# Optimization experiments

Hardware: AMD Instinct MI355X
Metric: run time of the kernel (lower is better)

Reference implementation:

```python
import jax, jax.numpy as jnp
import numpy as np


def setup_inputs() -> dict:
    key = jax.random.key(0)
    k1, k2, k3 = jax.random.split(key, 3)
    B, C, Z, S, T, H = 8, 128, 4, 8, 1024, 64
    WQ = jax.random.normal(k1, (C, Z, S, H), dtype=jnp.float32)
    WK = jax.random.normal(k2, (B, Z, T, H), dtype=jnp.float32)
    K = jax.random.normal(k3, (B, Z, T, H), dtype=jnp.float32)
    return {"WQ": WQ, "WK": WK, "K": K}


def reference(WQ, WK, K):
    # tanh non-linearities on keys (WQ is used raw, as in the original)
    WKt = jnp.tanh(WK)          # [b,z,t,h]
    Kt = jnp.tanh(K)            # [b,z,t,h]
    # attention scores per (batch, code, group, synonym) over tokens t
    scores = jnp.einsum('bzth,czsh->bczst', WKt, WQ)   # [b,c,z,s,t]
    attn = jax.nn.softmax(scores, axis=-1)             # softmax over t
    # weighted sum of (tanh'd) values over tokens
    context = jnp.einsum('bzth,bczst->bczsh', Kt, attn)  # [b,c,z,s,h]
    # AvgPool3d((1, s, 1)) then squeeze(-2) == mean over synonym axis s
    context = jnp.mean(context, axis=3)                  # [b,c,z,h]
    return (scores, context, attn)
```

## Files before the change

kernel.cpp:

```cpp
#include <hip/hip_runtime.h>

typedef _Float16 f16;
typedef f16 f16x4 __attribute__((ext_vector_type(4)));
typedef f16 f16x8 __attribute__((ext_vector_type(8)));
typedef float f32x16 __attribute__((ext_vector_type(16)));

#define NB 8
#define NC 128
#define NZ 4
#define NS 8
#define NT 1024
#define NH 64

#define WQ_N (NC*NZ*NS*NH)
#define WK_N (NB*NZ*NT*NH)

#define OUT_CTX  (NB*NC*NZ*NS*NT)
#define OUT_ATTN (OUT_CTX + NB*NC*NZ*NH)

__device__ __forceinline__ float fast_tanh(float x) {
    float e = __expf(2.0f * x);
    return 1.0f - 2.0f * __builtin_amdgcn_rcpf(e + 1.0f);
}

__global__ __launch_bounds__(256) void prep_kernel(
    const float* __restrict__ WQ, const float* __restrict__ WK, const float* __restrict__ K,
    f16* __restrict__ wqh, f16* __restrict__ wkh, f16* __restrict__ ktT)
{
    __shared__ f16 ldsT[64*64];
    const int tid = threadIdx.x;
    const int blk = blockIdx.x;
    if (blk < 512) {
        const int bz = blk >> 4;
        const int t0 = (blk & 15) << 6;
        #pragma unroll
        for (int it = 0; it < 4; ++it) {
            int idx = it*256 + tid;
            int tl  = idx >> 4;
            int seg = idx & 15;
            int gi  = (bz*NT + t0 + tl)*NH + seg*4;
            float4 wk4 = *(const float4*)(WK + gi);
            float4 k4  = *(const float4*)(K  + gi);
            f16x4 wv;
            wv[0] = (f16)fast_tanh(wk4.x);
            wv[1] = (f16)fast_tanh(wk4.y);
            wv[2] = (f16)fast_tanh(wk4.z);
            wv[3] = (f16)fast_tanh(wk4.w);
            *(f16x4*)(wkh + gi) = wv;
            ldsT[(seg*4+0)*64 + tl] = (f16)fast_tanh(k4.x);
            ldsT[(seg*4+1)*64 + tl] = (f16)fast_tanh(k4.y);
            ldsT[(seg*4+2)*64 + tl] = (f16)fast_tanh(k4.z);
            ldsT[(seg*4+3)*64 + tl] = (f16)fast_tanh(k4.w);
        }
        __syncthreads();
        #pragma unroll
        for (int it = 0; it < 4; ++it) {
            int idx = it*256 + tid;
            int h  = idx >> 4;
            int ts = idx & 15;
            f16x4 v = *(const f16x4*)&ldsT[h*64 + ts*4];
            *(f16x4*)(ktT + (bz*NH + h)*NT + t0 + ts*4) = v;
        }
    } else {
        const int ib = blk - 512;
        #pragma unroll
        for (int it = 0; it < 16; ++it) {
            int gi = ib*16384 + it*1024 + tid*4;
            float4 q = *(const float4*)(WQ + gi);
            f16x4 w;
            w[0] = (f16)q.x; w[1] = (f16)q.y; w[2] = (f16)q.z; w[3] = (f16)q.w;
            *(f16x4*)(wqh + gi) = w;
        }
    }
}

__global__ __launch_bounds__(256, 2) void fused_kernel(
    const f16* __restrict__ wqh, const f16* __restrict__ wkh, const f16* __restrict__ ktT,
    float* __restrict__ scores, float* __restrict__ attn, float* __restrict__ ctxout)
{
    __shared__ float rsL[4][32];
    __shared__ float invL[32];
    __shared__ f16   attnB[4][1024];
    __shared__ float ctxW[4][32][64];

    const int tid  = threadIdx.x;
    const int wave = tid >> 6;
    const int lane = tid & 63;
    const int l31  = lane & 31;
    const int g    = lane >> 5;
    const int bid  = blockIdx.x;
    const int bz = bid & 31, mt = bid >> 5;
    const int b = bz >> 2, z = bz & 3;
    const int m0 = mt * 32;

    const int mgA = m0 + l31;
    const f16* ap = wqh + (((mgA >> 3)*NZ + z)*NS + (mgA & 7))*NH + g*8;
    f16x8 afr[4];
    #pragma unroll
    for (int st = 0; st < 4; ++st) afr[st] = *(const f16x8*)(ap + st*16);

    f32x16 acc[8];
    #pragma unroll
    for (int tt = 0; tt < 8; ++tt)
        #pragma unroll
        for (int r = 0; r < 16; ++r) acc[tt][r] = 0.f;

    #pragma unroll
    for (int tt = 0; tt < 8; ++tt) {
        const int t0 = (tt*4 + wave) * 32;
        const f16* bp = wkh + (bz*NT + t0 + l31)*NH + g*8;
        #pragma unroll
        for (int st = 0; st < 4; ++st) {
            f16x8 bfr = *(const f16x8*)(bp + st*16);
            acc[tt] = __builtin_amdgcn_mfma_f32_32x32x16_f16(afr[st], bfr, acc[tt], 0, 0, 0);
        }
    }

    const int base2 = ((b*NC + mt*4)*NZ + z)*NS*NT;
    float p[16];
    #pragma unroll
    for (int r = 0; r < 16; ++r) p[r] = 0.f;

    #pragma unroll
    for (int tt = 0; tt < 8; ++tt) {
        const int tcol = (tt*4 + wave)*32 + l31;
        #pragma unroll
        for (int r = 0; r < 16; ++r) {
            int off = base2 + (r >> 2)*32768 + ((r & 3) + 4*g)*1024 + tcol;
            float v = acc[tt][r];
            scores[off] = v;
            p[r] += __expf(v);
        }
    }

    #pragma unroll
    for (int d = 1; d < 32; d <<= 1)
        #pragma unroll
        for (int r = 0; r < 16; ++r) p[r] += __shfl_xor(p[r], d, 64);

    if (l31 == 0) {
        #pragma unroll
        for (int r = 0; r < 16; ++r) rsL[wave][(r & 3) + 8*(r >> 2) + 4*g] = p[r];
    }
    __syncthreads();
    if (tid < 32) invL[tid] = 1.0f / (rsL[0][tid] + rsL[1][tid] + rsL[2][tid] + rsL[3][tid]);
    __syncthreads();

    f32x16 cacc[2];
    #pragma unroll
    for (int nt = 0; nt < 2; ++nt)
        #pragma unroll
        for (int r = 0; r < 16; ++r) cacc[nt][r] = 0.f;

    #pragma unroll
    for (int tt = 0; tt < 8; ++tt) {
        const int t0 = (tt*4 + wave) * 32;
        const int tcol = t0 + l31;
        f16x8 bfr2[2][2];
        #pragma unroll
        for (int s2 = 0; s2 < 2; ++s2)
            #pragma unroll
            for (int nt = 0; nt < 2; ++nt)
                bfr2[s2][nt] = *(const f16x8*)(ktT + (bz*NH + nt*32 + l31)*NT + t0 + s2*16 + g*8);

        #pragma unroll
        for (int r = 0; r < 16; ++r) {
            int ml = (r & 3) + 8*(r >> 2) + 4*g;
            float a = __expf(acc[tt][r]) * invL[ml];
            int off = base2 + (r >> 2)*32768 + ((r & 3) + 4*g)*1024 + tcol;
            attn[off] = a;
            int tb = l31 >> 3;
            int ai = ((tb*32 + ml)*8 + (l31 & 7)) ^ (tb << 3);
            attnB[wave][ai] = (f16)a;
        }
        #pragma unroll
        for (int s2 = 0; s2 < 2; ++s2) {
            int tb = 2*s2 + g;
            int ai = ((tb*32 + l31)*8) ^ (tb << 3);
            f16x8 pa = *(const f16x8*)&attnB[wave][ai];
            #pragma unroll
            for (int nt = 0; nt < 2; ++nt)
                cacc[nt] = __builtin_amdgcn_mfma_f32_32x32x16_f16(pa, bfr2[s2][nt], cacc[nt], 0, 0, 0);
        }
    }

    #pragma unroll
    for (int nt = 0; nt < 2; ++nt) {
        #pragma unroll
        for (int r = 0; r < 16; ++r) {
            int ml = (r & 3) + 8*(r >> 2) + 4*g;
            ctxW[wave][ml][nt*32 + l31] = cacc[nt][r];
        }
    }
    __syncthreads();

    {
        int cl = tid >> 6;
        int h  = tid & 63;
        float sum = 0.f;
        #pragma unroll
        for (int w = 0; w < 4; ++w)
            #pragma unroll
            for (int q = 0; q < 8; ++q)
                sum += ctxW[w][cl*8 + q][h];
        ctxout[((b*NC + (m0 >> 3) + cl)*NZ + z)*NH + h] = sum * 0.125f;
    }
}

extern "C" void kernel_launch(void* const* d_in, const int* in_sizes, int n_in,
                              void* d_out, int out_size, void* d_ws, size_t ws_size,
                              hipStream_t stream)
{
    const float* WQ = (const float*)d_in[0];
    const float* WK = (const float*)d_in[1];
    const float* K  = (const float*)d_in[2];

    char* ws = (char*)d_ws;
    f16* wqh = (f16*)(ws);
    f16* wkh = (f16*)(ws + (size_t)WQ_N*2);
    f16* ktT = (f16*)(ws + (size_t)WQ_N*2 + (size_t)WK_N*2);

    float* out    = (float*)d_out;
    float* scores = out;
    float* ctxout = out + OUT_CTX;
    float* attn   = out + OUT_ATTN;

    hipLaunchKernelGGL(prep_kernel, dim3(528), dim3(256), 0, stream,
                       WQ, WK, K, wqh, wkh, ktT);
    hipLaunchKernelGGL(fused_kernel, dim3(1024), dim3(256), 0, stream,
                       wqh, wkh, ktT, scores, attn, ctxout);
}
```

Measured before the change: 69.68 us.

## Stage scores and attn tiles through LDS for coalesced float4 global stores

Score and attention values are now written to a per-wave, double-buffered, XOR-swizzled LDS tile and read back as float4 rows, so each global store is a contiguous 16-byte vector instead of a scattered 4-byte write. Each wave now owns a contiguous 256-token range rather than an interleaved one, which makes the 32-token tile rows contiguous in memory. The cost is 32KB of extra shared memory per block, which may cut occupancy. Synchronization between lanes relies only on an LDS waitcnt with no barrier.

```diff
diff --git a/kernel.cpp b/kernel.cpp
--- a/kernel.cpp
+++ b/kernel.cpp
@@ -80,6 +80,7 @@
 {
     __shared__ float rsL[4][32];
     __shared__ float invL[32];
+    __shared__ float tileT[4][2][1024];
     __shared__ f16   attnB[4][1024];
     __shared__ float ctxW[4][32][64];
 
@@ -93,6 +94,10 @@
     const int b = bz >> 2, z = bz & 3;
     const int m0 = mt * 32;
 
+    const int srow = lane >> 3;
+    const int scol = (lane & 7) * 4;
+    const int sxor = scol ^ (srow << 2);
+
     const int mgA = m0 + l31;
     const f16* ap = wqh + (((mgA >> 3)*NZ + z)*NS + (mgA & 7))*NH + g*8;
     f16x8 afr[4];
@@ -107,7 +112,7 @@
 
     #pragma unroll
     for (int tt = 0; tt < 8; ++tt) {
-        const int t0 = (tt*4 + wave) * 32;
+        const int t0 = (wave*8 + tt) * 32;
         const f16* bp = wkh + (bz*NT + t0 + l31)*NH + g*8;
         #pragma unroll
         for (int st = 0; st < 4; ++st) {
@@ -123,13 +128,19 @@
 
     #pragma unroll
     for (int tt = 0; tt < 8; ++tt) {
-        const int tcol = (tt*4 + wave)*32 + l31;
+        const int t0 = (wave*8 + tt) * 32;
+        float* tb = tileT[wave][tt & 1];
         #pragma unroll
         for (int r = 0; r < 16; ++r) {
-            int off = base2 + (r >> 2)*32768 + ((r & 3) + 4*g)*1024 + tcol;
-            float v = acc[tt][r];
-            scores[off] = v;
-            p[r] += __expf(v);
+            int ml = (r & 3) + 8*(r >> 2) + 4*g;
+            tb[ml*32 + (l31 ^ (((r & 3) + 4*g) << 2))] = acc[tt][r];
+            p[r] += __expf(acc[tt][r]);
+        }
+        __builtin_amdgcn_s_waitcnt(0xc07f);
+        #pragma unroll
+        for (int q = 0; q < 4; ++q) {
+            float4 v = *(float4*)&tb[(q*8 + srow)*32 + sxor];
+            *(float4*)(scores + base2 + q*32768 + srow*1024 + t0 + scol) = v;
         }
     }
 
@@ -154,8 +165,7 @@
 
     #pragma unroll
     for (int tt = 0; tt < 8; ++tt) {
-        const int t0 = (tt*4 + wave) * 32;
-        const int tcol = t0 + l31;
+        const int t0 = (wave*8 + tt) * 32;
         f16x8 bfr2[2][2];
         #pragma unroll
         for (int s2 = 0; s2 < 2; ++s2)
@@ -163,20 +173,26 @@
             for (int nt = 0; nt < 2; ++nt)
                 bfr2[s2][nt] = *(const f16x8*)(ktT + (bz*NH + nt*32 + l31)*NT + t0 + s2*16 + g*8);
 
+        float* tb = tileT[wave][tt & 1];
         #pragma unroll
         for (int r = 0; r < 16; ++r) {
             int ml = (r & 3) + 8*(r >> 2) + 4*g;
             float a = __expf(acc[tt][r]) * invL[ml];
-            int off = base2 + (r >> 2)*32768 + ((r & 3) + 4*g)*1024 + tcol;
-            attn[off] = a;
-            int tb = l31 >> 3;
-            int ai = ((tb*32 + ml)*8 + (l31 & 7)) ^ (tb << 3);
+            tb[ml*32 + (l31 ^ (((r & 3) + 4*g) << 2))] = a;
+            int tbk = l31 >> 3;
+            int ai = ((tbk*32 + ml)*8 + (l31 & 7)) ^ (tbk << 3);
             attnB[wave][ai] = (f16)a;
         }
+        __builtin_amdgcn_s_waitcnt(0xc07f);
+        #pragma unroll
+        for (int q = 0; q < 4; ++q) {
+            float4 v = *(float4*)&tb[(q*8 + srow)*32 + sxor];
+            *(float4*)(attn + base2 + q*32768 + srow*1024 + t0 + scol) = v;
+        }
         #pragma unroll
         for (int s2 = 0; s2 < 2; ++s2) {
-            int tb = 2*s2 + g;
-            int ai = ((tb*32 + l31)*8) ^ (tb << 3);
+            int tbk = 2*s2 + g;
+            int ai = ((tbk*32 + l31)*8) ^ (tbk << 3);
             f16x8 pa = *(const f16x8*)&attnB[wave][ai];
             #pragma unroll
             for (int nt = 0; nt < 2; ++nt)
```

New measurement: 69.42 us (median of 2 runs). No clear change (-0.4%).

## Split fused softmax kernel into scores and recompute attn-PV kernels for occupancy

Applied to the files above, without the earlier changes.

Splits the fused kernel into two. The first computes scores, writes them, and stores per-row inverse softmax sums to workspace. The second recomputes the QK^T tile per token chunk, then applies exp and the inverse sum and runs the PV MFMA. It no longer keeps eight accumulator tiles live in registers and reuses the context scratch LDS for attention staging, so both kernels can declare 4 blocks per CU. In exchange the QK matmul runs twice, WK is read twice, and there is one more launch. Token assignment per wave also changes to contiguous chunks.

```diff
diff --git a/kernel.cpp b/kernel.cpp
--- a/kernel.cpp
+++ b/kernel.cpp
@@ -74,15 +74,11 @@
     }
 }
 
-__global__ __launch_bounds__(256, 2) void fused_kernel(
-    const f16* __restrict__ wqh, const f16* __restrict__ wkh, const f16* __restrict__ ktT,
-    float* __restrict__ scores, float* __restrict__ attn, float* __restrict__ ctxout)
+__global__ __launch_bounds__(256, 4) void scores_kernel(
+    const f16* __restrict__ wqh, const f16* __restrict__ wkh,
+    float* __restrict__ scores, float* __restrict__ invws)
 {
     __shared__ float rsL[4][32];
-    __shared__ float invL[32];
-    __shared__ f16   attnB[4][1024];
-    __shared__ float ctxW[4][32][64];
-
     const int tid  = threadIdx.x;
     const int wave = tid >> 6;
     const int lane = tid & 63;
@@ -99,63 +95,86 @@
     #pragma unroll
     for (int st = 0; st < 4; ++st) afr[st] = *(const f16x8*)(ap + st*16);
 
-    f32x16 acc[8];
-    #pragma unroll
-    for (int tt = 0; tt < 8; ++tt)
-        #pragma unroll
-        for (int r = 0; r < 16; ++r) acc[tt][r] = 0.f;
+    const int base2 = ((b*NC + mt*4)*NZ + z)*NS*NT;
+    float p[16];
+    #pragma unroll
+    for (int r = 0; r < 16; ++r) p[r] = 0.f;
+
+    f32x16 accD[2];
 
     #pragma unroll
     for (int tt = 0; tt < 8; ++tt) {
-        const int t0 = (tt*4 + wave) * 32;
+        const int t0 = (wave*8 + tt) * 32;
         const f16* bp = wkh + (bz*NT + t0 + l31)*NH + g*8;
+        #pragma unroll
+        for (int r = 0; r < 16; ++r) accD[tt & 1][r] = 0.f;
         #pragma unroll
         for (int st = 0; st < 4; ++st) {
             f16x8 bfr = *(const f16x8*)(bp + st*16);
-            acc[tt] = __builtin_amdgcn_mfma_f32_32x32x16_f16(afr[st], bfr, acc[tt], 0, 0, 0);
-        }
-    }
+            accD[tt & 1] = __builtin_amdgcn_mfma_f32_32x32x16_f16(afr[st], bfr, accD[tt & 1], 0, 0, 0);
+        }
+        const int tcol = t0 + l31;
+        #pragma unroll
+        for (int r = 0; r < 16; ++r) {
+            float v = accD[tt & 1][r];
+            scores[base2 + (r >> 2)*32768 + ((r & 3) + 4*g)*1024 + tcol] = v;
+            p[r] += __expf(v);
+        }
+    }
+
+    #pragma unroll
+    for (int d = 1; d < 32; d <<= 1)
+        #pragma unroll
+        for (int r = 0; r < 16; ++r) p[r] += __shfl_xor(p[r], d, 64);
+
+    if (l31 == 0) {
+        #pragma unroll
+        for (int r = 0; r < 16; ++r) rsL[wave][(r & 3) + 8*(r >> 2) + 4*g] = p[r];
+    }
+    __syncthreads();
+    if (tid < 32) invws[bz*1024 + m0 + tid] =
+        1.0f / (rsL[0][tid] + rsL[1][tid] + rsL[2][tid] + rsL[3][tid]);
+}
+
+__global__ __launch_bounds__(256, 4) void attn_pv_kernel(
+    const f16* __restrict__ wqh, const f16* __restrict__ wkh, const f16* __restrict__ ktT,
+    const float* __restrict__ invws, float* __restrict__ attn, float* __restrict__ ctxout)
+{
+    __shared__ float ctxW[4][32][64];
+    __shared__ float invL[32];
+
+    const int tid  = threadIdx.x;
+    const int wave = tid >> 6;
+    const int lane = tid & 63;
+    const int l31  = lane & 31;
+    const int g    = lane >> 5;
+    const int bid  = blockIdx.x;
+    const int bz = bid & 31, mt = bid >> 5;
+    const int b = bz >> 2, z = bz & 3;
+    const int m0 = mt * 32;
+
+    f16* attnB = (f16*)&ctxW[wave][0][0];
+
+    if (tid < 32) invL[tid] = invws[bz*1024 + m0 + tid];
+    __syncthreads();
+
+    const int mgA = m0 + l31;
+    const f16* ap = wqh + (((mgA >> 3)*NZ + z)*NS + (mgA & 7))*NH + g*8;
+    f16x8 afr[4];
+    #pragma unroll
+    for (int st = 0; st < 4; ++st) afr[st] = *(const f16x8*)(ap + st*16);
 
     const int base2 = ((b*NC + mt*4)*NZ + z)*NS*NT;
-    float p[16];
-    #pragma unroll
-    for (int r = 0; r < 16; ++r) p[r] = 0.f;
+
+    f32x16 cacc[2];
+    #pragma unroll
+    for (int nt = 0; nt < 2; ++nt)
+        #pragma unroll
+        for (int r = 0; r < 16; ++r) cacc[nt][r] = 0.f;
 
     #pragma unroll
     for (int tt = 0; tt < 8; ++tt) {
-        const int tcol = (tt*4 + wave)*32 + l31;
-        #pragma unroll
-        for (int r = 0; r < 16; ++r) {
-            int off = base2 + (r >> 2)*32768 + ((r & 3) + 4*g)*1024 + tcol;
-            float v = acc[tt][r];
-            scores[off] = v;
-            p[r] += __expf(v);
-        }
-    }
-
-    #pragma unroll
-    for (int d = 1; d < 32; d <<= 1)
-        #pragma unroll
-        for (int r = 0; r < 16; ++r) p[r] += __shfl_xor(p[r], d, 64);
-
-    if (l31 == 0) {
-        #pragma unroll
-        for (int r = 0; r < 16; ++r) rsL[wave][(r & 3) + 8*(r >> 2) + 4*g] = p[r];
-    }
-    __syncthreads();
-    if (tid < 32) invL[tid] = 1.0f / (rsL[0][tid] + rsL[1][tid] + rsL[2][tid] + rsL[3][tid]);
-    __syncthreads();
-
-    f32x16 cacc[2];
-    #pragma unroll
-    for (int nt = 0; nt < 2; ++nt)
-        #pragma unroll
-        for (int r = 0; r < 16; ++r) cacc[nt][r] = 0.f;
-
-    #pragma unroll
-    for (int tt = 0; tt < 8; ++tt) {
-        const int t0 = (tt*4 + wave) * 32;
-        const int tcol = t0 + l31;
+        const int t0 = (wave*8 + tt) * 32;
         f16x8 bfr2[2][2];
         #pragma unroll
         for (int s2 = 0; s2 < 2; ++s2)
@@ -163,26 +182,38 @@
             for (int nt = 0; nt < 2; ++nt)
                 bfr2[s2][nt] = *(const f16x8*)(ktT + (bz*NH + nt*32 + l31)*NT + t0 + s2*16 + g*8);
 
+        const f16* bp = wkh + (bz*NT + t0 + l31)*NH + g*8;
+        f32x16 acc;
+        #pragma unroll
+        for (int r = 0; r < 16; ++r) acc[r] = 0.f;
+        #pragma unroll
+        for (int st = 0; st < 4; ++st) {
+            f16x8 bfr = *(const f16x8*)(bp + st*16);
+            acc = __builtin_amdgcn_mfma_f32_32x32x16_f16(afr[st], bfr, acc, 0, 0, 0);
+        }
+
+        const int tcol = t0 + l31;
         #pragma unroll
         for (int r = 0; r < 16; ++r) {
             int ml = (r & 3) + 8*(r >> 2) + 4*g;
-            float a = __expf(acc[tt][r]) * invL[ml];
-            int off = base2 + (r >> 2)*32768 + ((r & 3) + 4*g)*1024 + tcol;
-            attn[off] = a;
-            int tb = l31 >> 3;
-            int ai = ((tb*32 + ml)*8 + (l31 & 7)) ^ (tb << 3);
-            attnB[wave][ai] = (f16)a;
+            float a = __expf(acc[r]) * invL[ml];
+            attn[base2 + (r >> 2)*32768 + ((r & 3) + 4*g)*1024 + tcol] = a;
+            int tbk = l31 >> 3;
+            int ai = ((tbk*32 + ml)*8 + (l31 & 7)) ^ (tbk << 3);
+            attnB[ai] = (f16)a;
         }
         #pragma unroll
         for (int s2 = 0; s2 < 2; ++s2) {
-            int tb = 2*s2 + g;
-            int ai = ((tb*32 + l31)*8) ^ (tb << 3);
-            f16x8 pa = *(const f16x8*)&attnB[wave][ai];
+            int tbk = 2*s2 + g;
+            int ai = ((tbk*32 + l31)*8) ^ (tbk << 3);
+            f16x8 pa = *(const f16x8*)&attnB[ai];
             #pragma unroll
             for (int nt = 0; nt < 2; ++nt)
                 cacc[nt] = __builtin_amdgcn_mfma_f32_32x32x16_f16(pa, bfr2[s2][nt], cacc[nt], 0, 0, 0);
         }
     }
+
+    __syncthreads();
 
     #pragma unroll
     for (int nt = 0; nt < 2; ++nt) {
@@ -219,6 +250,7 @@
     f16* wqh = (f16*)(ws);
     f16* wkh = (f16*)(ws + (size_t)WQ_N*2);
     f16* ktT = (f16*)(ws + (size_t)WQ_N*2 + (size_t)WK_N*2);
+    float* invws = (float*)(ws + (size_t)WQ_N*2 + (size_t)WK_N*4);
 
     float* out    = (float*)d_out;
     float* scores = out;
@@ -227,6 +259,8 @@
 
     hipLaunchKernelGGL(prep_kernel, dim3(528), dim3(256), 0, stream,
                        WQ, WK, K, wqh, wkh, ktT);
-    hipLaunchKernelGGL(fused_kernel, dim3(1024), dim3(256), 0, stream,
-                       wqh, wkh, ktT, scores, attn, ctxout);
-}
+    hipLaunchKernelGGL(scores_kernel, dim3(1024), dim3(256), 0, stream,
+                       wqh, wkh, scores, invws);
+    hipLaunchKernelGGL(attn_pv_kernel, dim3(1024), dim3(256), 0, stream,
+                       wqh, wkh, ktT, invws, attn, ctxout);
+}
```

After: 184.3 us. 164% more time.
